# Optimization experiments

Measured on AMD Instinct MI355X. Metric: run time of the kernel, lower is better.

Reference implementation:

```python
import jax, jax.numpy as jnp
import numpy as np

B, S, D = 4, 2048, 1024
E, H, TOP_K = 8, 4096, 2


def setup_inputs() -> dict:
    key = jax.random.key(0)
    ks = jax.random.split(key, 5)
    scale = 0.02
    return {
        "x": jax.random.normal(ks[0], (B, S, D), dtype=jnp.float32),
        "Wr": jax.random.normal(ks[1], (D, E), dtype=jnp.float32) * scale,
        "br": jnp.zeros((E,), dtype=jnp.float32),
        "W1": jax.random.normal(ks[2], (E, D, H), dtype=jnp.float32) * scale,
        "b1": jnp.zeros((E, H), dtype=jnp.float32),
        "W2": jax.random.normal(ks[3], (E, H, D), dtype=jnp.float32) * scale,
        "b2": jnp.zeros((E, D), dtype=jnp.float32),
    }


def reference(x, Wr, br, W1, b1, W2, b2):
    b, s, d = x.shape
    xf = x.reshape(-1, d)                                   # [T, D]
    gate = jax.nn.softmax(xf @ Wr + br, axis=-1)            # [T, E]
    top_w, top_i = jax.lax.top_k(gate, TOP_K)               # [T, K]
    top_w = top_w / jnp.sum(top_w, axis=-1, keepdims=True)
    # combine[t, e] = sum_i top_w[t, i] * 1{top_i[t, i] == e}
    combine = jnp.sum(jax.nn.one_hot(top_i, E, dtype=xf.dtype) * top_w[..., None], axis=1)  # [T, E]
    # Dense all-expert FFN (same math as the masked per-expert loops in torch)
    h = jax.nn.gelu(jnp.einsum('td,edh->teh', xf, W1) + b1, approximate=False)  # [T, E, H]
    out = jnp.einsum('teh,ehd,te->td', h, W2, combine) + combine @ b2           # [T, D]
    return out.reshape(b, s, d)
```

## Files before the change

### kernel.cpp

```cpp
#include <hip/hip_runtime.h>
#include <cstdio>


#define T_TOK 8192
#define DIM   1024
#define NEXP  8
#define HID   4096
#define MAXR  18432

typedef float          f32x4   __attribute__((ext_vector_type(4)));
typedef short          bf16x8  __attribute__((ext_vector_type(8)));
typedef unsigned short u16x8   __attribute__((ext_vector_type(8)));
typedef unsigned short u16x4   __attribute__((ext_vector_type(4)));

static __device__ __forceinline__ unsigned short f2bf(float f) {
  unsigned int u = __builtin_bit_cast(unsigned int, f);
  u = (u + 0x7FFFu + ((u >> 16) & 1u)) >> 16;
  return (unsigned short)u;
}

static __device__ __forceinline__ void gl16(const void* g, void* l) {
  __builtin_amdgcn_global_load_lds(
      (const __attribute__((address_space(1))) unsigned int*)g,
      (__attribute__((address_space(3))) unsigned int*)l,
      16, 0, 0);
}

static __device__ __forceinline__ void transpose_body(const float* __restrict__ W,
                                                      unsigned short* __restrict__ WT,
                                                      int R, int C, int bx, int by, int e) {
  int lane = threadIdx.x & 63, w = threadIdx.x >> 6;
  int r0 = by * 64, c0 = bx * 128 + w * 32;
  int r8 = (lane & 7) * 8, cg = lane >> 3;
  const float* src = W + (size_t)e * R * C + (size_t)(r0 + r8) * C + c0 + cg * 4;
  float4 v[8];
#pragma unroll
  for (int j = 0; j < 8; ++j) v[j] = *(const float4*)(src + (size_t)j * C);
  unsigned short* dst = WT + (size_t)e * R * C + (size_t)(c0 + cg * 4) * R + r0 + r8;
#pragma unroll
  for (int s = 0; s < 4; ++s) {
    u16x8 o;
#pragma unroll
    for (int j = 0; j < 8; ++j) {
      float f = s == 0 ? v[j].x : s == 1 ? v[j].y : s == 2 ? v[j].z : v[j].w;
      o[j] = f2bf(f);
    }
    *(u16x8*)(dst + (size_t)s * R) = o;
  }
}

static __device__ __forceinline__ void router_body(int blk, const float* __restrict__ x,
                                                   const float* __restrict__ Wr,
                                                   const float* __restrict__ br,
                                                   int* __restrict__ meta,
                                                   int2* __restrict__ top_i,
                                                   float2* __restrict__ top_w) {
  int lane = threadIdx.x & 63;
  int wid  = threadIdx.x >> 6;
  int t = blk * 4 + wid;
  const float* xp = x + (size_t)t * DIM + lane * 16;
  float acc[NEXP];
#pragma unroll
  for (int e = 0; e < NEXP; ++e) acc[e] = 0.f;
#pragma unroll
  for (int j = 0; j < 16; j += 4) {
    float4 xv = *(const float4*)(xp + j);
    const float* wp = Wr + (size_t)(lane * 16 + j) * NEXP;
#pragma unroll
    for (int jj = 0; jj < 4; ++jj) {
      float xs = jj == 0 ? xv.x : jj == 1 ? xv.y : jj == 2 ? xv.z : xv.w;
      float4 w0 = *(const float4*)(wp + jj * NEXP);
      float4 w1 = *(const float4*)(wp + jj * NEXP + 4);
      acc[0] += xs * w0.x; acc[1] += xs * w0.y; acc[2] += xs * w0.z; acc[3] += xs * w0.w;
      acc[4] += xs * w1.x; acc[5] += xs * w1.y; acc[6] += xs * w1.z; acc[7] += xs * w1.w;
    }
  }
#pragma unroll
  for (int off = 32; off > 0; off >>= 1) {
#pragma unroll
    for (int e = 0; e < NEXP; ++e) acc[e] += __shfl_xor(acc[e], off);
  }
  if (lane == 0) {
    float l[NEXP];
#pragma unroll
    for (int e = 0; e < NEXP; ++e) l[e] = acc[e] + br[e];
    int e1 = 0;
#pragma unroll
    for (int e = 1; e < NEXP; ++e) if (l[e] > l[e1]) e1 = e;
    int e2 = (e1 == 0) ? 1 : 0;
#pragma unroll
    for (int e = 0; e < NEXP; ++e) if (e != e1 && l[e] > l[e2]) e2 = e;
    float g  = expf(l[e2] - l[e1]);
    float w1 = 1.f / (1.f + g);
    top_i[t] = make_int2(e1, e2);
    top_w[t] = make_float2(w1, 1.f - w1);
    atomicAdd(&meta[e1], 1);
    atomicAdd(&meta[e2], 1);
  }
}

__global__ __launch_bounds__(256) void prep_k(const float* __restrict__ W1,
                                              const float* __restrict__ W2,
                                              unsigned short* __restrict__ W1bT,
                                              unsigned short* __restrict__ W2bT,
                                              const float* __restrict__ x,
                                              const float* __restrict__ Wr,
                                              const float* __restrict__ br,
                                              int* __restrict__ meta,
                                              int2* __restrict__ top_i,
                                              float2* __restrict__ top_w,
                                              int* __restrict__ tok_of_row,
                                              float* __restrict__ wt_of_row) {
  int id = blockIdx.x;
  if (id < 4096) {
    int rem = id & 511;
    transpose_body(W1, W1bT, DIM, HID, rem & 31, rem >> 5, id >> 9);
  } else if (id < 8192) {
    int id2 = id - 4096;
    int rem = id2 & 511;
    transpose_body(W2, W2bT, HID, DIM, rem & 7, rem >> 3, id2 >> 9);
  } else if (id < 10240) {
    router_body(id - 8192, x, Wr, br, meta, top_i, top_w);
  } else {
    int i = (id - 10240) * 256 + threadIdx.x;
    if (i < MAXR) { tok_of_row[i] = 0; wt_of_row[i] = 0.f; }
  }
}

__global__ void prefix_k(int* __restrict__ meta) {
  if (threadIdx.x == 0) {
    int s = 0;
#pragma unroll
    for (int e = 0; e < NEXP; ++e) {
      meta[16 + e] = s;
      s += (meta[e] + 255) & ~255;
    }
    meta[24] = s;
    meta[25] = s;
  }
}

__global__ __launch_bounds__(256) void scatter_k(const int2* __restrict__ top_i,
                                                 const float2* __restrict__ top_w,
                                                 int* __restrict__ meta,
                                                 int* __restrict__ row_of,
                                                 int* __restrict__ tok_of_row,
                                                 float* __restrict__ wt_of_row) {
  int t = blockIdx.x * 256 + threadIdx.x;
  int2  ei = top_i[t];
  float2 w = top_w[t];
  int p = atomicAdd(&meta[8 + ei.x], 1);
  int r = meta[16 + ei.x] + p;
  tok_of_row[r] = t; wt_of_row[r] = w.x; row_of[t * 2] = r;
  p = atomicAdd(&meta[8 + ei.y], 1);
  r = meta[16 + ei.y] + p;
  tok_of_row[r] = t; wt_of_row[r] = w.y; row_of[t * 2 + 1] = r;
}

__global__ __launch_bounds__(256) void gather_k(const float* __restrict__ x,
                                                const int* __restrict__ tok_of_row,
                                                const int* __restrict__ meta,
                                                unsigned short* __restrict__ xg) {
  int r = blockIdx.x;
  if (r >= meta[25]) return;
  int t = tok_of_row[r];
  int c = threadIdx.x * 4;
  float4 v = *(const float4*)(x + (size_t)t * DIM + c);
  u16x4 o;
  o[0] = f2bf(v.x); o[1] = f2bf(v.y); o[2] = f2bf(v.z); o[3] = f2bf(v.w);
  *(u16x4*)(xg + (size_t)r * DIM + c) = o;
}


template <int KTOT, int NTOT, int EPI>
__global__ __launch_bounds__(256, 4) void gemmv10_k(const unsigned short* __restrict__ A,
                                                    const unsigned short* __restrict__ Bt,
                                                    const float* __restrict__ bias,
                                                    const int* __restrict__ meta,
                                                    const float* __restrict__ wt_of_row,
                                                    const int* __restrict__ tok_of_row,
                                                    void* __restrict__ Cout) {
  constexpr int NN  = NTOT / 128;
  constexpr int NXB = MAXR / 128;
  constexpr int NWG = NXB * NN;
  constexpr int NSR = NXB / 4;
  constexpr int NKT = KTOT / 32;
  __shared__ __align__(16) unsigned short lds[8192];

  int id = ((int)blockIdx.x & 7) * (NWG / 8) + ((int)blockIdx.x >> 3);
  int sid = id >> 4, sub = id & 15;
  int row0 = ((sid % NSR) * 4 + (sub & 3)) * 128;
  int n0   = ((sid / NSR) * 4 + (sub >> 2)) * 128;
  if (row0 >= meta[25]) return;
  int e = 0;
  while (meta[17 + e] <= row0) ++e;
  if (row0 - meta[16 + e] >= meta[e]) return;
  const unsigned short* Bp = Bt + (size_t)e * NTOT * KTOT;

  int tid = threadIdx.x;
  int lane = tid & 63, wid = tid >> 6;
  int wm = wid >> 1, wn = wid & 1;

  int s = (tid & 3) ^ ((tid >> 3) & 3);
  const unsigned short* pA0 = A + (size_t)(row0 + (tid >> 2)) * KTOT + s * 8;
  const unsigned short* pA1 = pA0 + (size_t)64 * KTOT;
  const unsigned short* pB0 = Bp + (size_t)(n0 + (tid >> 2)) * KTOT + s * 8;
  const unsigned short* pB1 = pB0 + (size_t)64 * KTOT;

  int am = lane & 15;
  int sF = ((lane >> 4) ^ ((lane >> 1) & 3)) * 8;
  int aoff = (wm * 64 + am) * 32 + sF;
  int boff = 4096 + (wn * 64 + am) * 32 + sF;

  f32x4 acc[4][4];
#pragma unroll
  for (int i = 0; i < 4; ++i)
#pragma unroll
    for (int j = 0; j < 4; ++j) acc[i][j] = (f32x4){0.f, 0.f, 0.f, 0.f};

  for (int kt = 0; kt < NKT; ++kt) {
    __syncthreads();
    gl16(pA0 + kt * 32, lds + tid * 8);
    gl16(pA1 + kt * 32, lds + 2048 + tid * 8);
    gl16(pB0 + kt * 32, lds + 4096 + tid * 8);
    gl16(pB1 + kt * 32, lds + 6144 + tid * 8);
    __syncthreads();
    bf16x8 af[4], bv[4];
#pragma unroll
    for (int i = 0; i < 4; ++i)
      af[i] = *(const bf16x8*)(lds + aoff + i * 512);
#pragma unroll
    for (int j = 0; j < 4; ++j)
      bv[j] = *(const bf16x8*)(lds + boff + j * 512);
#pragma unroll
    for (int i = 0; i < 4; ++i)
#pragma unroll
      for (int j = 0; j < 4; ++j)
        acc[i][j] = __builtin_amdgcn_mfma_f32_16x16x32_bf16(af[i], bv[j], acc[i][j], 0, 0, 0);
  }

  int rbase = row0 + wm * 64 + ((lane >> 4) << 2);
  int nbase = n0 + wn * 64 + am;
  if constexpr (EPI == 0) {
    unsigned short* Hp = (unsigned short*)Cout;
    const float* bp = bias + (size_t)e * NTOT;
#pragma unroll
    for (int i = 0; i < 4; ++i)
#pragma unroll
      for (int j = 0; j < 4; ++j) {
        int n = nbase + j * 16;
        float bv = bp[n];
#pragma unroll
        for (int g = 0; g < 4; ++g) {
          int m = rbase + i * 16 + g;
          float v = acc[i][j][g] + bv;
          v = 0.5f * v * (1.f + erff(v * 0.70710678118654752f));
          Hp[(size_t)m * NTOT + n] = f2bf(v);
        }
      }
  } else {
    float* Op = (float*)Cout;
    const float* bp = bias + (size_t)e * NTOT;
#pragma unroll
    for (int i = 0; i < 4; ++i)
#pragma unroll
      for (int g = 0; g < 4; ++g) {
        int m = rbase + i * 16 + g;
        float wt = wt_of_row[m];
        if (wt != 0.f) {
          float* orow = Op + (size_t)tok_of_row[m] * DIM;
#pragma unroll
          for (int j = 0; j < 4; ++j) {
            int n = nbase + j * 16;
            atomicAdd(orow + n, (acc[i][j][g] + bp[n]) * wt);
          }
        }
      }
  }
}

extern "C" void kernel_launch(void* const* d_in, const int* in_sizes, int n_in,
                              void* d_out, int out_size, void* d_ws, size_t ws_size,
                              hipStream_t stream) {
  const float* x  = (const float*)d_in[0];
  const float* Wr = (const float*)d_in[1];
  const float* br = (const float*)d_in[2];
  const float* W1 = (const float*)d_in[3];
  const float* b1 = (const float*)d_in[4];
  const float* W2 = (const float*)d_in[5];
  const float* b2 = (const float*)d_in[6];
  float* out = (float*)d_out;

  char* base = (char*)d_ws;
  size_t off = 0;
  auto carve = [&](size_t bytes) -> void* {
    void* r = base + off;
    off = (off + bytes + 255) & ~(size_t)255;
    return r;
  };
  int*            meta       = (int*)carve(26 * 4);
  int2*           top_i      = (int2*)carve((size_t)T_TOK * 8);
  float2*         top_w      = (float2*)carve((size_t)T_TOK * 8);
  int*            row_of     = (int*)carve((size_t)T_TOK * 2 * 4);
  int*            tok_of_row = (int*)carve((size_t)MAXR * 4);
  float*          wt_of_row  = (float*)carve((size_t)MAXR * 4);
  unsigned short* xg         = (unsigned short*)carve((size_t)MAXR * DIM * 2);
  unsigned short* W1bT       = (unsigned short*)carve((size_t)NEXP * DIM * HID * 2);
  unsigned short* W2bT       = (unsigned short*)carve((size_t)NEXP * DIM * HID * 2);
  unsigned short* hbuf       = (unsigned short*)carve((size_t)MAXR * HID * 2);
  if (off > ws_size) {
    fprintf(stderr, "kernel_launch: ws_size too small: need %zu have %zu\n", off, ws_size);
    return;
  }

  hipMemsetAsync(meta, 0, 26 * 4, stream);
  hipMemsetAsync(out, 0, (size_t)out_size * 4, stream);
  hipLaunchKernelGGL(prep_k, dim3(10312), dim3(256), 0, stream,
                     W1, W2, W1bT, W2bT, x, Wr, br, meta, top_i, top_w,
                     tok_of_row, wt_of_row);
  hipLaunchKernelGGL(prefix_k, dim3(1), dim3(64), 0, stream, meta);
  hipLaunchKernelGGL(scatter_k, dim3(T_TOK / 256), dim3(256), 0, stream,
                     top_i, top_w, meta, row_of, tok_of_row, wt_of_row);
  hipLaunchKernelGGL(gather_k, dim3(MAXR), dim3(256), 0, stream, x, tok_of_row, meta, xg);
  hipLaunchKernelGGL((gemmv10_k<DIM, HID, 0>), dim3((MAXR / 128) * (HID / 128)), dim3(256), 0,
                     stream, xg, W1bT, b1, meta, wt_of_row, tok_of_row, (void*)hbuf);
  hipLaunchKernelGGL((gemmv10_k<HID, DIM, 1>), dim3((MAXR / 128) * (DIM / 128)), dim3(256), 0,
                     stream, hbuf, W2bT, b2, meta, wt_of_row, tok_of_row, (void*)out);
}
```

Baseline: 866.6 us.

## Reduce expert row padding to 128 and simplify GEMM tile mapping

Per-expert row groups are now padded to multiples of 128 instead of 256, and the maximum row count shrinks accordingly, so fewer empty padding tiles are computed. The GEMM kernel drops the grouped 4x4 tile raster for a plain row-major mapping and removes the XOR swizzle on LDS loads and fragment reads. It also drops the occupancy hint in launch_bounds. The unswizzled LDS layout risks bank conflicts on fragment reads, and the simpler raster may reduce L2 reuse of weight tiles.

```diff
diff --git a/kernel.cpp b/kernel.cpp
--- a/kernel.cpp
+++ b/kernel.cpp
@@ -6,7 +6,7 @@
 #define DIM   1024
 #define NEXP  8
 #define HID   4096
-#define MAXR  18432
+#define MAXR  17408
 
 typedef float          f32x4   __attribute__((ext_vector_type(4)));
 typedef short          bf16x8  __attribute__((ext_vector_type(8)));
@@ -133,7 +133,7 @@
 #pragma unroll
     for (int e = 0; e < NEXP; ++e) {
       meta[16 + e] = s;
-      s += (meta[e] + 255) & ~255;
+      s += (meta[e] + 127) & ~127;
     }
     meta[24] = s;
     meta[25] = s;
@@ -173,24 +173,21 @@
 
 
 template <int KTOT, int NTOT, int EPI>
-__global__ __launch_bounds__(256, 4) void gemmv10_k(const unsigned short* __restrict__ A,
-                                                    const unsigned short* __restrict__ Bt,
-                                                    const float* __restrict__ bias,
-                                                    const int* __restrict__ meta,
-                                                    const float* __restrict__ wt_of_row,
-                                                    const int* __restrict__ tok_of_row,
-                                                    void* __restrict__ Cout) {
-  constexpr int NN  = NTOT / 128;
+__global__ __launch_bounds__(256) void gemmv11_k(const unsigned short* __restrict__ A,
+                                                 const unsigned short* __restrict__ Bt,
+                                                 const float* __restrict__ bias,
+                                                 const int* __restrict__ meta,
+                                                 const float* __restrict__ wt_of_row,
+                                                 const int* __restrict__ tok_of_row,
+                                                 void* __restrict__ Cout) {
   constexpr int NXB = MAXR / 128;
-  constexpr int NWG = NXB * NN;
-  constexpr int NSR = NXB / 4;
+  constexpr int NWG = NXB * (NTOT / 128);
   constexpr int NKT = KTOT / 32;
   __shared__ __align__(16) unsigned short lds[8192];
 
   int id = ((int)blockIdx.x & 7) * (NWG / 8) + ((int)blockIdx.x >> 3);
-  int sid = id >> 4, sub = id & 15;
-  int row0 = ((sid % NSR) * 4 + (sub & 3)) * 128;
-  int n0   = ((sid / NSR) * 4 + (sub >> 2)) * 128;
+  int row0 = (id % NXB) * 128;
+  int n0   = (id / NXB) * 128;
   if (row0 >= meta[25]) return;
   int e = 0;
   while (meta[17 + e] <= row0) ++e;
@@ -200,17 +197,13 @@
   int tid = threadIdx.x;
   int lane = tid & 63, wid = tid >> 6;
   int wm = wid >> 1, wn = wid & 1;
-
-  int s = (tid & 3) ^ ((tid >> 3) & 3);
-  const unsigned short* pA0 = A + (size_t)(row0 + (tid >> 2)) * KTOT + s * 8;
-  const unsigned short* pA1 = pA0 + (size_t)64 * KTOT;
-  const unsigned short* pB0 = Bp + (size_t)(n0 + (tid >> 2)) * KTOT + s * 8;
-  const unsigned short* pB1 = pB0 + (size_t)64 * KTOT;
-
-  int am = lane & 15;
-  int sF = ((lane >> 4) ^ ((lane >> 1) & 3)) * 8;
-  int aoff = (wm * 64 + am) * 32 + sF;
-  int boff = 4096 + (wn * 64 + am) * 32 + sF;
+  int rs = tid >> 2;
+  int cs = (tid & 3) * 8;
+
+  const unsigned short* Ag = A  + (size_t)(row0 + rs) * KTOT + cs;
+  const unsigned short* Bg = Bp + (size_t)(n0   + rs) * KTOT + cs;
+  unsigned short* Al = lds + tid * 8;
+  unsigned short* Bl = lds + 4096 + tid * 8;
 
   f32x4 acc[4][4];
 #pragma unroll
@@ -218,20 +211,22 @@
 #pragma unroll
     for (int j = 0; j < 4; ++j) acc[i][j] = (f32x4){0.f, 0.f, 0.f, 0.f};
 
-  for (int kt = 0; kt < NKT; ++kt) {
+  int am = lane & 15, ak = (lane >> 4) * 8;
+
+  for (int kt = 0; kt < KTOT; kt += 32) {
     __syncthreads();
-    gl16(pA0 + kt * 32, lds + tid * 8);
-    gl16(pA1 + kt * 32, lds + 2048 + tid * 8);
-    gl16(pB0 + kt * 32, lds + 4096 + tid * 8);
-    gl16(pB1 + kt * 32, lds + 6144 + tid * 8);
+    gl16(Ag + kt, Al);
+    gl16(Ag + 64 * KTOT + kt, Al + 2048);
+    gl16(Bg + kt, Bl);
+    gl16(Bg + 64 * KTOT + kt, Bl + 2048);
     __syncthreads();
     bf16x8 af[4], bv[4];
 #pragma unroll
     for (int i = 0; i < 4; ++i)
-      af[i] = *(const bf16x8*)(lds + aoff + i * 512);
+      af[i] = *(const bf16x8*)(lds + (wm * 64 + i * 16 + am) * 32 + ak);
 #pragma unroll
     for (int j = 0; j < 4; ++j)
-      bv[j] = *(const bf16x8*)(lds + boff + j * 512);
+      bv[j] = *(const bf16x8*)(lds + 4096 + (wn * 64 + j * 16 + am) * 32 + ak);
 #pragma unroll
     for (int i = 0; i < 4; ++i)
 #pragma unroll
@@ -315,15 +310,15 @@
 
   hipMemsetAsync(meta, 0, 26 * 4, stream);
   hipMemsetAsync(out, 0, (size_t)out_size * 4, stream);
-  hipLaunchKernelGGL(prep_k, dim3(10312), dim3(256), 0, stream,
+  hipLaunchKernelGGL(prep_k, dim3(10308), dim3(256), 0, stream,
                      W1, W2, W1bT, W2bT, x, Wr, br, meta, top_i, top_w,
                      tok_of_row, wt_of_row);
   hipLaunchKernelGGL(prefix_k, dim3(1), dim3(64), 0, stream, meta);
   hipLaunchKernelGGL(scatter_k, dim3(T_TOK / 256), dim3(256), 0, stream,
                      top_i, top_w, meta, row_of, tok_of_row, wt_of_row);
   hipLaunchKernelGGL(gather_k, dim3(MAXR), dim3(256), 0, stream, x, tok_of_row, meta, xg);
-  hipLaunchKernelGGL((gemmv10_k<DIM, HID, 0>), dim3((MAXR / 128) * (HID / 128)), dim3(256), 0,
+  hipLaunchKernelGGL((gemmv11_k<DIM, HID, 0>), dim3((MAXR / 128) * (HID / 128)), dim3(256), 0,
                      stream, xg, W1bT, b1, meta, wt_of_row, tok_of_row, (void*)hbuf);
-  hipLaunchKernelGGL((gemmv10_k<HID, DIM, 1>), dim3((MAXR / 128) * (DIM / 128)), dim3(256), 0,
+  hipLaunchKernelGGL((gemmv11_k<HID, DIM, 1>), dim3((MAXR / 128) * (DIM / 128)), dim3(256), 0,
                      stream, hbuf, W2bT, b2, meta, wt_of_row, tok_of_row, (void*)out);
 }
```

Result: slower. 936.9 us (+8.1%).
